# Kernel tuning notes

Hardware: AMD Instinct MI355X
Metric: run time of the kernel (lower is better)

The kernel has to match this reference:

```python
import jax, jax.numpy as jnp
import numpy as np

N_USER = 60082   # n_fields: size of station/field table
N_STATION = 14695
D = 128
B = 8
K = 32


def setup_inputs() -> dict:
    key = jax.random.key(0)
    ks = jax.random.split(key, 20)
    inp = {
        'user_embedding': jax.random.normal(ks[0], (B, D), jnp.float32),
        'station_embedding': jax.random.normal(ks[1], (N_USER, D), jnp.float32),
        'raw_field_embed': jax.random.normal(ks[2], (N_USER, D), jnp.float32),
        'his_nodes': jax.random.randint(ks[3], (B, K), 0, N_USER),
        'now_nodes': jax.random.randint(ks[4], (B, K), 0, N_USER),
        'user_id': jax.random.randint(ks[5], (B,), 0, N_STATION),
        # learned parameters
        'user_emb_table': jax.random.normal(ks[6], (N_STATION, D), jnp.float32) * 0.02,
        'station_emb_table': jax.random.normal(ks[7], (N_USER, D), jnp.float32) * 0.02,
        'proj_w': jax.random.normal(ks[8], (D, D), jnp.float32) / np.sqrt(D),
        'proj_b': jnp.zeros((D,), jnp.float32),
        'theta': jax.random.uniform(ks[9], (N_STATION, 1), jnp.float32),
        'alpha': jax.random.uniform(ks[10], (N_USER, 1), jnp.float32),
        'w_his1': jax.random.normal(ks[11], (D, D // 2), jnp.float32) / np.sqrt(D),
        'b_his1': jnp.zeros((D // 2,), jnp.float32),
        'w_his2': jax.random.normal(ks[12], (D // 2, D), jnp.float32) / np.sqrt(D // 2),
        'b_his2': jnp.zeros((D,), jnp.float32),
        'w_st': jax.random.normal(ks[13], (D, 1), jnp.float32) / np.sqrt(D),
        'b_st': jnp.zeros((1,), jnp.float32),
        'w_u': jax.random.normal(ks[14], (D, 1), jnp.float32) / np.sqrt(D),
        'b_u': jnp.zeros((1,), jnp.float32),
    }
    return inp


def reference(user_embedding, station_embedding, raw_field_embed,
              user_emb_table, station_emb_table, proj_w, proj_b,
              theta, alpha, w_his1, b_his1, w_his2, b_his2,
              w_st, b_st, w_u, b_u,
              his_nodes, now_nodes, user_id):
    # user_mem_stat: gated mix of dynamic and static user embedding (dropout = eval identity)
    th = theta[user_id]                                    # [B,1]
    user_mem = (1.0 - th) * user_embedding + th * user_emb_table[user_id]  # [B,D]

    # full-table projection, shared across batch (the torch loop recomputes it)
    proj = station_emb_table @ proj_w + proj_b             # [N,D]

    b_idx = jnp.arange(B)[:, None]                         # [B,1]
    beta = jnp.zeros((B, N_USER), user_embedding.dtype)
    beta = beta.at[b_idx, now_nodes].set(1.0)
    beta = beta.at[b_idx, his_nodes].set(1.0)              # use_his=True path

    embed = (1.0 - beta[..., None] * alpha[None]) * proj[None]  # [B,N,D]

    # scatter-add current-node contribution
    now_add = alpha[now_nodes] * station_embedding[now_nodes]  # [B,K,D]
    embed = embed.at[b_idx, now_nodes].add(now_add)

    # history MLP (Linear -> LeakyReLU -> Linear) on gathered raw field embeds
    h = raw_field_embed[his_nodes]                         # [B,K,D]
    h = jax.nn.leaky_relu(h @ w_his1 + b_his1) @ w_his2 + b_his2
    embed = embed.at[b_idx, his_nodes].add(alpha[his_nodes] * h)

    station_out = (embed @ w_st)[..., 0] + b_st[0]         # [B,N]
    user_out = user_mem @ w_u + b_u                        # [B,1]
    return station_out + user_out                          # [B,N]
```

## Files before the change

### kernel.cpp

```cpp
#include <hip/hip_runtime.h>

#define NU 60082
#define NST 14695
#define D 128
#define B 8
#define K 32
#define NBLK ((NU + 63) / 64)

__global__ __launch_bounds__(256) void k_fused(
    const float* __restrict__ user_embedding,
    const float* __restrict__ station_embedding,
    const float* __restrict__ raw_field_embed,
    const int* __restrict__ his_nodes,
    const int* __restrict__ now_nodes,
    const int* __restrict__ user_id,
    const float* __restrict__ user_emb_table,
    const float* __restrict__ station_emb_table,
    const float* __restrict__ proj_w,
    const float* __restrict__ proj_b,
    const float* __restrict__ theta,
    const float* __restrict__ alpha,
    const float* __restrict__ w_his1,
    const float* __restrict__ b_his1,
    const float* __restrict__ w_his2,
    const float* __restrict__ b_his2,
    const float* __restrict__ w_st,
    const float* __restrict__ b_st,
    const float* __restrict__ w_u,
    const float* __restrict__ b_u,
    float* __restrict__ out)
{
    __shared__ float s_wst[128];
    __shared__ float s_v[128];
    __shared__ float s_v2[64];
    __shared__ float s_tile[64];
    __shared__ float s_uc[8];
    __shared__ unsigned char s_flag[8 * 64];
    __shared__ short s_lslot[512];
    __shared__ int   s_lnode[512];
    __shared__ float s_lval[512];
    __shared__ int   s_cnt, s_hcnt;
    __shared__ float s_c, s_c2;

    const int t  = threadIdx.x;
    const int sb = blockIdx.x;
    const int row0 = sb * 64;

    const int w    = t >> 6;
    const int lane = t & 63;
    const int half = lane >> 5;
    const int l32  = lane & 31;

    if (t < 32) ((float4*)s_wst)[t] = ((const float4*)w_st)[t];
    if (t >= 64 && t < 192) ((int*)s_flag)[t - 64] = 0;
    if (t == 192) s_cnt = 0;
    if (t == 193) s_hcnt = 0;

    float4 xr[8];
    #pragma unroll
    for (int i = 0; i < 8; ++i) {
        int r = i * 8 + w * 2 + half;
        int row = row0 + r;
        if (row < NU)
            xr[i] = ((const float4*)(station_emb_table + (size_t)row * D))[l32];
        else
            xr[i] = make_float4(0.f, 0.f, 0.f, 0.f);
    }
    __syncthreads();

    if (t < 128) {
        float acc = 0.f;
        const float4* pr = (const float4*)(proj_w + t * D);
        #pragma unroll 8
        for (int j = 0; j < 32; ++j) {
            float4 x = pr[j];
            float4 wv = ((float4*)s_wst)[j];
            acc += x.x * wv.x + x.y * wv.y + x.z * wv.z + x.w * wv.w;
        }
        s_v[t] = acc;
    } else if (t < 160) {
        int l = t - 128;
        float4 x = ((const float4*)proj_b)[l];
        float4 wv = ((float4*)s_wst)[l];
        float p = x.x * wv.x + x.y * wv.y + x.z * wv.z + x.w * wv.w;
        #pragma unroll
        for (int off = 16; off >= 1; off >>= 1) p += __shfl_down(p, off, 32);
        if (l == 0) s_c = p;
    } else if (t < 192) {
        int l = t - 160;
        float4 x = ((const float4*)b_his2)[l];
        float4 wv = ((float4*)s_wst)[l];
        float p = x.x * wv.x + x.y * wv.y + x.z * wv.z + x.w * wv.w;
        #pragma unroll
        for (int off = 16; off >= 1; off >>= 1) p += __shfl_down(p, off, 32);
        if (l == 0) s_c2 = p;
    }

    {
        int n0 = now_nodes[t];
        if ((n0 >> 6) == sb) {
            s_flag[(t >> 5) * 64 + (n0 & 63)] = 1;
            int i = atomicAdd(&s_cnt, 1);
            s_lslot[i] = (short)t;
            s_lnode[i] = n0;
        }
        int n1 = his_nodes[t];
        if ((n1 >> 6) == sb) {
            s_flag[(t >> 5) * 64 + (n1 & 63)] = 1;
            int i = atomicAdd(&s_cnt, 1);
            s_lslot[i] = (short)(256 + t);
            s_lnode[i] = n1;
            atomicAdd(&s_hcnt, 1);
        }
    }
    {
        int u = t >> 5, l = t & 31;
        int uid = user_id[u];
        float th = theta[uid];
        float4 ue = ((const float4*)(user_embedding + u * D))[l];
        float4 ut = ((const float4*)(user_emb_table + (size_t)uid * D))[l];
        float4 wu = ((const float4*)w_u)[l];
        float p = ((1.f - th) * ue.x + th * ut.x) * wu.x
                + ((1.f - th) * ue.y + th * ut.y) * wu.y
                + ((1.f - th) * ue.z + th * ut.z) * wu.z
                + ((1.f - th) * ue.w + th * ut.w) * wu.w;
        #pragma unroll
        for (int off = 16; off >= 1; off >>= 1) p += __shfl_down(p, off, 32);
        if (l == 0) s_uc[u] = p + b_u[0] + b_st[0];
    }
    __syncthreads();

    const int cnt  = s_cnt;
    const int hcnt = s_hcnt;

    const float4 vv = ((const float4*)s_v)[l32];
    const float  c  = s_c;
    #pragma unroll
    for (int i = 0; i < 8; ++i) {
        int r = i * 8 + w * 2 + half;
        float acc = xr[i].x * vv.x + xr[i].y * vv.y + xr[i].z * vv.z + xr[i].w * vv.w;
        #pragma unroll
        for (int off = 16; off >= 1; off >>= 1) acc += __shfl_down(acc, off, 32);
        if (l32 == 0) s_tile[r] = acc + c;
    }
    __syncthreads();

    {
        const int nl = t & 63;
        const int b0 = t >> 6;
        const int row = row0 + nl;
        if (row < NU) {
            float sv = s_tile[nl];
            if (!s_flag[b0 * 64 + nl])
                out[(size_t)b0 * NU + row] = sv + s_uc[b0];
            if (!s_flag[(b0 + 4) * 64 + nl])
                out[(size_t)(b0 + 4) * NU + row] = sv + s_uc[b0 + 4];
        }
    }

    if (cnt > 0) {
        if (hcnt > 0) {
            int row = t >> 2, q = t & 3;
            const float4* wr = (const float4*)(w_his2 + row * D);
            float p = 0.f;
            #pragma unroll
            for (int i = 0; i < 8; ++i) {
                float4 x = wr[q + 4 * i];
                float4 wv = ((float4*)s_wst)[q + 4 * i];
                p += x.x * wv.x + x.y * wv.y + x.z * wv.z + x.w * wv.w;
            }
            p += __shfl_down(p, 2, 4);
            p += __shfl_down(p, 1, 4);
            if (q == 0) s_v2[row] = p;
        }
        __syncthreads();

        for (int i = w; i < cnt; i += 4) {
            int slot = s_lslot[i];
            int n = s_lnode[i];
            float val;
            if (slot < 256) {
                const float* se = station_embedding + (size_t)n * D;
                float p = se[lane] * s_wst[lane] + se[64 + lane] * s_wst[64 + lane];
                #pragma unroll
                for (int off = 32; off >= 1; off >>= 1) p += __shfl_down(p, off, 64);
                val = alpha[n] * p;
            } else {
                const float4* rf = (const float4*)(raw_field_embed + (size_t)n * D);
                float h1 = b_his1[lane];
                #pragma unroll 8
                for (int j = 0; j < 32; ++j) {
                    float4 r = rf[j];
                    h1 += r.x * w_his1[(4 * j + 0) * 64 + lane]
                        + r.y * w_his1[(4 * j + 1) * 64 + lane]
                        + r.z * w_his1[(4 * j + 2) * 64 + lane]
                        + r.w * w_his1[(4 * j + 3) * 64 + lane];
                }
                float ha = h1 > 0.f ? h1 : 0.01f * h1;
                float p = ha * s_v2[lane];
                #pragma unroll
                for (int off = 32; off >= 1; off >>= 1) p += __shfl_down(p, off, 64);
                val = alpha[n] * (p + s_c2);
            }
            if (lane == 0) s_lval[i] = val;
        }
        __syncthreads();

        if (t < cnt) {
            int n = s_lnode[t];
            int b = (s_lslot[t] & 255) >> 5;
            bool first = true;
            for (int i = 0; i < t; ++i)
                if (s_lnode[i] == n && ((s_lslot[i] & 255) >> 5) == b) { first = false; break; }
            if (first) {
                float sum = 0.f;
                for (int i = 0; i < cnt; ++i)
                    if (s_lnode[i] == n && ((s_lslot[i] & 255) >> 5) == b) sum += s_lval[i];
                out[(size_t)b * NU + n] = (1.f - alpha[n]) * s_tile[n - row0] + s_uc[b] + sum;
            }
        }
    }
}

extern "C" void kernel_launch(void* const* d_in, const int* in_sizes, int n_in,
                              void* d_out, int out_size, void* d_ws, size_t ws_size,
                              hipStream_t stream) {
    const float* user_embedding    = (const float*)d_in[0];
    const float* station_embedding = (const float*)d_in[1];
    const float* raw_field_embed   = (const float*)d_in[2];
    const int*   his_nodes         = (const int*)d_in[3];
    const int*   now_nodes         = (const int*)d_in[4];
    const int*   user_id           = (const int*)d_in[5];
    const float* user_emb_table    = (const float*)d_in[6];
    const float* station_emb_table = (const float*)d_in[7];
    const float* proj_w            = (const float*)d_in[8];
    const float* proj_b            = (const float*)d_in[9];
    const float* theta             = (const float*)d_in[10];
    const float* alpha             = (const float*)d_in[11];
    const float* w_his1            = (const float*)d_in[12];
    const float* b_his1            = (const float*)d_in[13];
    const float* w_his2            = (const float*)d_in[14];
    const float* b_his2            = (const float*)d_in[15];
    const float* w_st              = (const float*)d_in[16];
    const float* b_st              = (const float*)d_in[17];
    const float* w_u               = (const float*)d_in[18];
    const float* b_u               = (const float*)d_in[19];
    float* out = (float*)d_out;

    hipLaunchKernelGGL(k_fused, dim3(NBLK), dim3(256), 0, stream,
                       user_embedding, station_embedding, raw_field_embed,
                       his_nodes, now_nodes, user_id, user_emb_table,
                       station_emb_table, proj_w, proj_b, theta, alpha,
                       w_his1, b_his1, w_his2, b_his2,
                       w_st, b_st, w_u, b_u, out);
}
```

Measured before the change: 156.3 us.

## Split into precompute kernel and streaming main kernel with shared-memory scatter-add

Moves the per-table projection vector, the user bias terms and the per-slot now and history contributions into a small 130-block pre-kernel that writes them to workspace. The main kernel then only streams the station table, reduces it against the precomputed vector and applies flagged adds accumulated in shared memory with atomics. This replaces the old per-block redundant proj_w reduction and the serial deduplication loop. It adds a second launch and a dependency on the workspace, and floating-point summation order for duplicate nodes now depends on atomic order.

```diff
diff --git a/kernel.cpp b/kernel.cpp
--- a/kernel.cpp
+++ b/kernel.cpp
@@ -7,7 +7,13 @@
 #define K 32
 #define NBLK ((NU + 63) / 64)
 
-__global__ __launch_bounds__(256) void k_fused(
+#define WS_V    0
+#define WS_C    128
+#define WS_UC   136
+#define WS_NOW  192
+#define WS_HIS  448
+
+__global__ __launch_bounds__(256) void k_pre(
     const float* __restrict__ user_embedding,
     const float* __restrict__ station_embedding,
     const float* __restrict__ raw_field_embed,
@@ -15,7 +21,6 @@
     const int* __restrict__ now_nodes,
     const int* __restrict__ user_id,
     const float* __restrict__ user_emb_table,
-    const float* __restrict__ station_emb_table,
     const float* __restrict__ proj_w,
     const float* __restrict__ proj_b,
     const float* __restrict__ theta,
@@ -28,92 +33,36 @@
     const float* __restrict__ b_st,
     const float* __restrict__ w_u,
     const float* __restrict__ b_u,
-    float* __restrict__ out)
+    float* __restrict__ ws)
 {
     __shared__ float s_wst[128];
-    __shared__ float s_v[128];
-    __shared__ float s_v2[64];
-    __shared__ float s_tile[64];
-    __shared__ float s_uc[8];
-    __shared__ unsigned char s_flag[8 * 64];
-    __shared__ short s_lslot[512];
-    __shared__ int   s_lnode[512];
-    __shared__ float s_lval[512];
-    __shared__ int   s_cnt, s_hcnt;
-    __shared__ float s_c, s_c2;
-
     const int t  = threadIdx.x;
-    const int sb = blockIdx.x;
-    const int row0 = sb * 64;
-
-    const int w    = t >> 6;
-    const int lane = t & 63;
-    const int half = lane >> 5;
-    const int l32  = lane & 31;
+    const int bb = blockIdx.x;
 
     if (t < 32) ((float4*)s_wst)[t] = ((const float4*)w_st)[t];
-    if (t >= 64 && t < 192) ((int*)s_flag)[t - 64] = 0;
-    if (t == 192) s_cnt = 0;
-    if (t == 193) s_hcnt = 0;
-
-    float4 xr[8];
-    #pragma unroll
-    for (int i = 0; i < 8; ++i) {
-        int r = i * 8 + w * 2 + half;
-        int row = row0 + r;
-        if (row < NU)
-            xr[i] = ((const float4*)(station_emb_table + (size_t)row * D))[l32];
-        else
-            xr[i] = make_float4(0.f, 0.f, 0.f, 0.f);
-    }
-    __syncthreads();
-
-    if (t < 128) {
-        float acc = 0.f;
-        const float4* pr = (const float4*)(proj_w + t * D);
-        #pragma unroll 8
-        for (int j = 0; j < 32; ++j) {
-            float4 x = pr[j];
-            float4 wv = ((float4*)s_wst)[j];
-            acc += x.x * wv.x + x.y * wv.y + x.z * wv.z + x.w * wv.w;
-        }
-        s_v[t] = acc;
-    } else if (t < 160) {
-        int l = t - 128;
-        float4 x = ((const float4*)proj_b)[l];
-        float4 wv = ((float4*)s_wst)[l];
-        float p = x.x * wv.x + x.y * wv.y + x.z * wv.z + x.w * wv.w;
-        #pragma unroll
-        for (int off = 16; off >= 1; off >>= 1) p += __shfl_down(p, off, 32);
-        if (l == 0) s_c = p;
-    } else if (t < 192) {
-        int l = t - 160;
-        float4 x = ((const float4*)b_his2)[l];
-        float4 wv = ((float4*)s_wst)[l];
-        float p = x.x * wv.x + x.y * wv.y + x.z * wv.z + x.w * wv.w;
-        #pragma unroll
-        for (int off = 16; off >= 1; off >>= 1) p += __shfl_down(p, off, 32);
-        if (l == 0) s_c2 = p;
-    }
-
-    {
-        int n0 = now_nodes[t];
-        if ((n0 >> 6) == sb) {
-            s_flag[(t >> 5) * 64 + (n0 & 63)] = 1;
-            int i = atomicAdd(&s_cnt, 1);
-            s_lslot[i] = (short)t;
-            s_lnode[i] = n0;
-        }
-        int n1 = his_nodes[t];
-        if ((n1 >> 6) == sb) {
-            s_flag[(t >> 5) * 64 + (n1 & 63)] = 1;
-            int i = atomicAdd(&s_cnt, 1);
-            s_lslot[i] = (short)(256 + t);
-            s_lnode[i] = n1;
-            atomicAdd(&s_hcnt, 1);
-        }
-    }
-    {
+    __syncthreads();
+
+    if (bb == 0) {
+        if (t < 128) {
+            float acc = 0.f;
+            const float4* pr = (const float4*)(proj_w + t * D);
+            #pragma unroll 8
+            for (int j = 0; j < 32; ++j) {
+                float4 x = pr[j];
+                float4 wv = ((float4*)s_wst)[j];
+                acc += x.x * wv.x + x.y * wv.y + x.z * wv.z + x.w * wv.w;
+            }
+            ws[WS_V + t] = acc;
+        } else if (t < 160) {
+            int l = t - 128;
+            float4 x = ((const float4*)proj_b)[l];
+            float4 wv = ((float4*)s_wst)[l];
+            float p = x.x * wv.x + x.y * wv.y + x.z * wv.z + x.w * wv.w;
+            #pragma unroll
+            for (int off = 16; off >= 1; off >>= 1) p += __shfl_down(p, off, 32);
+            if (l == 0) ws[WS_C] = p;
+        }
+    } else if (bb == 1) {
         int u = t >> 5, l = t & 31;
         int uid = user_id[u];
         float th = theta[uid];
@@ -126,98 +75,142 @@
                 + ((1.f - th) * ue.w + th * ut.w) * wu.w;
         #pragma unroll
         for (int off = 16; off >= 1; off >>= 1) p += __shfl_down(p, off, 32);
-        if (l == 0) s_uc[u] = p + b_u[0] + b_st[0];
-    }
-    __syncthreads();
-
-    const int cnt  = s_cnt;
-    const int hcnt = s_hcnt;
-
-    const float4 vv = ((const float4*)s_v)[l32];
-    const float  c  = s_c;
+        if (l == 0) ws[WS_UC + u] = p + b_u[0] + b_st[0];
+    } else if (bb < 66) {
+        int w = t >> 6, lane = t & 63;
+        int slot = (bb - 2) * 4 + w;
+        int n = now_nodes[slot];
+        const float* se = station_embedding + (size_t)n * D;
+        float p = se[lane] * s_wst[lane] + se[64 + lane] * s_wst[64 + lane];
+        #pragma unroll
+        for (int off = 32; off >= 1; off >>= 1) p += __shfl_down(p, off, 64);
+        if (lane == 0) ws[WS_NOW + slot] = alpha[n] * p;
+    } else {
+        int w = t >> 6, h = t & 63;
+        int slot = (bb - 66) * 4 + w;
+        int n = his_nodes[slot];
+        float v2h = 0.f;
+        const float4* wr = (const float4*)(w_his2 + h * D);
+        #pragma unroll 8
+        for (int j = 0; j < 32; ++j) {
+            float4 x = wr[j];
+            float4 wv = ((float4*)s_wst)[j];
+            v2h += x.x * wv.x + x.y * wv.y + x.z * wv.z + x.w * wv.w;
+        }
+        const float4* rf = (const float4*)(raw_field_embed + (size_t)n * D);
+        float h1 = b_his1[h];
+        #pragma unroll 8
+        for (int j = 0; j < 32; ++j) {
+            float4 r = rf[j];
+            h1 += r.x * w_his1[(4 * j + 0) * 64 + h]
+                + r.y * w_his1[(4 * j + 1) * 64 + h]
+                + r.z * w_his1[(4 * j + 2) * 64 + h]
+                + r.w * w_his1[(4 * j + 3) * 64 + h];
+        }
+        float ha = h1 > 0.f ? h1 : 0.01f * h1;
+        float p = ha * v2h + b_his2[h] * s_wst[h] + b_his2[64 + h] * s_wst[64 + h];
+        #pragma unroll
+        for (int off = 32; off >= 1; off >>= 1) p += __shfl_down(p, off, 64);
+        if (h == 0) ws[WS_HIS + slot] = alpha[n] * p;
+    }
+}
+
+__global__ __launch_bounds__(256) void k_main(
+    const float* __restrict__ station_emb_table,
+    const int* __restrict__ his_nodes,
+    const int* __restrict__ now_nodes,
+    const float* __restrict__ alpha,
+    const float* __restrict__ ws,
+    float* __restrict__ out)
+{
+    __shared__ float s_v[128];
+    __shared__ float s_tile[64];
+    __shared__ float s_uc[8];
+    __shared__ float s_c;
+    __shared__ float s_add[8 * 64];
+    __shared__ unsigned char s_flag[8 * 64];
+
+    const int t  = threadIdx.x;
+    const int sb = blockIdx.x;
+    const int row0 = sb * 64;
+    const int w    = t >> 6;
+    const int lane = t & 63;
+    const int half = lane >> 5;
+    const int l32  = lane & 31;
+
+    const int n0 = now_nodes[t];
+    const int n1 = his_nodes[t];
+    const float wn = ws[WS_NOW + t];
+    const float wh = ws[WS_HIS + t];
+    float4 vv4 = make_float4(0.f, 0.f, 0.f, 0.f);
+    float ucv = 0.f, cv = 0.f;
+    if (t < 32) vv4 = ((const float4*)(ws + WS_V))[t];
+    if (t < 8)  ucv = ws[WS_UC + t];
+    if (t == 8) cv  = ws[WS_C];
+
+    if (t < 128) {
+        ((float4*)s_add)[t] = make_float4(0.f, 0.f, 0.f, 0.f);
+        ((int*)s_flag)[t] = 0;
+    }
+    if (t < 32) ((float4*)s_v)[t] = vv4;
+    if (t < 8)  s_uc[t] = ucv;
+    if (t == 8) s_c = cv;
+
+    float4 xr[8];
     #pragma unroll
     for (int i = 0; i < 8; ++i) {
         int r = i * 8 + w * 2 + half;
-        float acc = xr[i].x * vv.x + xr[i].y * vv.y + xr[i].z * vv.z + xr[i].w * vv.w;
-        #pragma unroll
-        for (int off = 16; off >= 1; off >>= 1) acc += __shfl_down(acc, off, 32);
-        if (l32 == 0) s_tile[r] = acc + c;
+        int row = row0 + r;
+        if (row < NU)
+            xr[i] = ((const float4*)(station_emb_table + (size_t)row * D))[l32];
+        else
+            xr[i] = make_float4(0.f, 0.f, 0.f, 0.f);
     }
     __syncthreads();
 
     {
-        const int nl = t & 63;
-        const int b0 = t >> 6;
+        const int b = t >> 5;
+        if ((n0 >> 6) == sb) {
+            int idx = b * 64 + (n0 & 63);
+            s_flag[idx] = 1;
+            atomicAdd(&s_add[idx], wn);
+        }
+        if ((n1 >> 6) == sb) {
+            int idx = b * 64 + (n1 & 63);
+            s_flag[idx] = 1;
+            atomicAdd(&s_add[idx], wh);
+        }
+    }
+    __syncthreads();
+
+    {
+        const float4 vv = ((const float4*)s_v)[l32];
+        const float  c  = s_c;
+        #pragma unroll
+        for (int i = 0; i < 8; ++i) {
+            int r = i * 8 + w * 2 + half;
+            float acc = xr[i].x * vv.x + xr[i].y * vv.y + xr[i].z * vv.z + xr[i].w * vv.w;
+            #pragma unroll
+            for (int off = 16; off >= 1; off >>= 1) acc += __shfl_down(acc, off, 32);
+            if (l32 == 0) s_tile[r] = acc + c;
+        }
+    }
+    __syncthreads();
+
+    {
+        const int nl  = t & 63;
+        const int b0  = t >> 6;
         const int row = row0 + nl;
         if (row < NU) {
-            float sv = s_tile[nl];
-            if (!s_flag[b0 * 64 + nl])
-                out[(size_t)b0 * NU + row] = sv + s_uc[b0];
-            if (!s_flag[(b0 + 4) * 64 + nl])
-                out[(size_t)(b0 + 4) * NU + row] = sv + s_uc[b0 + 4];
-        }
-    }
-
-    if (cnt > 0) {
-        if (hcnt > 0) {
-            int row = t >> 2, q = t & 3;
-            const float4* wr = (const float4*)(w_his2 + row * D);
-            float p = 0.f;
-            #pragma unroll
-            for (int i = 0; i < 8; ++i) {
-                float4 x = wr[q + 4 * i];
-                float4 wv = ((float4*)s_wst)[q + 4 * i];
-                p += x.x * wv.x + x.y * wv.y + x.z * wv.z + x.w * wv.w;
-            }
-            p += __shfl_down(p, 2, 4);
-            p += __shfl_down(p, 1, 4);
-            if (q == 0) s_v2[row] = p;
-        }
-        __syncthreads();
-
-        for (int i = w; i < cnt; i += 4) {
-            int slot = s_lslot[i];
-            int n = s_lnode[i];
-            float val;
-            if (slot < 256) {
-                const float* se = station_embedding + (size_t)n * D;
-                float p = se[lane] * s_wst[lane] + se[64 + lane] * s_wst[64 + lane];
-                #pragma unroll
-                for (int off = 32; off >= 1; off >>= 1) p += __shfl_down(p, off, 64);
-                val = alpha[n] * p;
-            } else {
-                const float4* rf = (const float4*)(raw_field_embed + (size_t)n * D);
-                float h1 = b_his1[lane];
-                #pragma unroll 8
-                for (int j = 0; j < 32; ++j) {
-                    float4 r = rf[j];
-                    h1 += r.x * w_his1[(4 * j + 0) * 64 + lane]
-                        + r.y * w_his1[(4 * j + 1) * 64 + lane]
-                        + r.z * w_his1[(4 * j + 2) * 64 + lane]
-                        + r.w * w_his1[(4 * j + 3) * 64 + lane];
-                }
-                float ha = h1 > 0.f ? h1 : 0.01f * h1;
-                float p = ha * s_v2[lane];
-                #pragma unroll
-                for (int off = 32; off >= 1; off >>= 1) p += __shfl_down(p, off, 64);
-                val = alpha[n] * (p + s_c2);
-            }
-            if (lane == 0) s_lval[i] = val;
-        }
-        __syncthreads();
-
-        if (t < cnt) {
-            int n = s_lnode[t];
-            int b = (s_lslot[t] & 255) >> 5;
-            bool first = true;
-            for (int i = 0; i < t; ++i)
-                if (s_lnode[i] == n && ((s_lslot[i] & 255) >> 5) == b) { first = false; break; }
-            if (first) {
-                float sum = 0.f;
-                for (int i = 0; i < cnt; ++i)
-                    if (s_lnode[i] == n && ((s_lslot[i] & 255) >> 5) == b) sum += s_lval[i];
-                out[(size_t)b * NU + n] = (1.f - alpha[n]) * s_tile[n - row0] + s_uc[b] + sum;
-            }
+            const float sv = s_tile[nl];
+            const int f0 = s_flag[b0 * 64 + nl];
+            const int f1 = s_flag[(b0 + 4) * 64 + nl];
+            float a = 0.f;
+            if (f0 | f1) a = alpha[row];
+            const float o0 = f0 ? sv * (1.f - a) + s_add[b0 * 64 + nl]       : sv;
+            const float o1 = f1 ? sv * (1.f - a) + s_add[(b0 + 4) * 64 + nl] : sv;
+            out[(size_t)b0 * NU + row]       = o0 + s_uc[b0];
+            out[(size_t)(b0 + 4) * NU + row] = o1 + s_uc[b0 + 4];
         }
     }
 }
@@ -246,11 +239,15 @@
     const float* w_u               = (const float*)d_in[18];
     const float* b_u               = (const float*)d_in[19];
     float* out = (float*)d_out;
-
-    hipLaunchKernelGGL(k_fused, dim3(NBLK), dim3(256), 0, stream,
+    float* ws  = (float*)d_ws;
+
+    hipLaunchKernelGGL(k_pre, dim3(130), dim3(256), 0, stream,
                        user_embedding, station_embedding, raw_field_embed,
                        his_nodes, now_nodes, user_id, user_emb_table,
-                       station_emb_table, proj_w, proj_b, theta, alpha,
+                       proj_w, proj_b, theta, alpha,
                        w_his1, b_his1, w_his2, b_his2,
-                       w_st, b_st, w_u, b_u, out);
+                       w_st, b_st, w_u, b_u, ws);
+
+    hipLaunchKernelGGL(k_main, dim3(NBLK), dim3(256), 0, stream,
+                       station_emb_table, his_nodes, now_nodes, alpha, ws, out);
 }
```

New measurement: 153.3 us (median of 2 runs). No clear change (-1.9%).
